# Kernel tuning notes

Hardware: AMD Instinct MI355X
Metric: run time of the kernel (lower is better)

Reference implementation:

```python
import jax, jax.numpy as jnp
import numpy as np

N_NODES = 50000
N_EDGES = 500000
H = 128          # h_dim
HEADS = 3
B = 512          # histories with non-zero length
L = 10           # seq_len (all histories full length)
N_RELS = 200
NEG_SLOPE = 0.2  # DGL GATConv default negative_slope


def setup_inputs() -> dict:
    key = jax.random.key(0)
    ks = jax.random.split(key, 18)
    p = lambda i, shape: jax.random.normal(ks[i], shape, jnp.float32) * 0.05
    return {
        "node_feat": jax.random.normal(ks[0], (N_NODES, H), jnp.float32),
        "W1": p(1, (H, HEADS * H)),
        "attn_l1": p(2, (HEADS, H)),
        "attn_r1": p(3, (HEADS, H)),
        "b1": p(4, (HEADS * H,)),
        "W2": p(5, (H, HEADS * H)),
        "attn_l2": p(6, (HEADS, H)),
        "attn_r2": p(7, (HEADS, H)),
        "b2": p(8, (HEADS * H,)),
        "ent_embeds": jax.random.normal(ks[9], (N_NODES, H), jnp.float32),
        "rel_embeds": jax.random.normal(ks[10], (N_RELS, H), jnp.float32),
        "global_emb_list": jax.random.normal(ks[11], (B * L, H), jnp.float32),
        "s_hist_t": jax.random.uniform(ks[12], (B, L), jnp.float32),
        "edge_src": jax.random.randint(ks[13], (N_EDGES,), 0, N_NODES),
        "edge_dst": jax.random.randint(ks[14], (N_EDGES,), 0, N_NODES),
        "node_ids_graph": jax.random.randint(ks[15], (B * L,), 0, N_NODES),
        "s_tem": jax.random.randint(ks[16], (B,), 0, N_NODES),
        "r_tem": jax.random.randint(ks[17], (B,), 0, N_RELS),
    }


def gat_conv(x, W, attn_l, attn_r, bias, src, dst):
    """DGL-style GATConv (allow_zero_in_degree=True, eval mode)."""
    n = x.shape[0]
    feat = (x @ W).reshape(n, HEADS, H)                    # [N, heads, H]
    el = jnp.einsum('nhd,hd->nh', feat, attn_l)            # [N, heads]
    er = jnp.einsum('nhd,hd->nh', feat, attn_r)
    e = jax.nn.leaky_relu(el[src] + er[dst], NEG_SLOPE)    # [E, heads]
    # edge softmax over incoming edges of each dst node
    emax = jax.ops.segment_max(e, dst, num_segments=n)
    ex = jnp.exp(e - emax[dst])
    denom = jax.ops.segment_sum(ex, dst, num_segments=n)
    alpha = ex / denom[dst]                                # [E, heads]
    msg = alpha[:, :, None] * feat[src]                    # [E, heads, H]
    rst = jax.ops.segment_sum(msg, dst, num_segments=n)    # [N, heads, H]
    return rst + bias.reshape(1, HEADS, H)


def reference(node_feat, W1, attn_l1, attn_r1, b1, W2, attn_l2, attn_r2, b2,
              ent_embeds, rel_embeds, global_emb_list, s_hist_t,
              edge_src, edge_dst, node_ids_graph, s_tem, r_tem):
    h = gat_conv(node_feat, W1, attn_l1, attn_r1, b1, edge_src, edge_dst).mean(axis=1)
    h = gat_conv(h, W2, attn_l2, attn_r2, b2, edge_src, edge_dst).mean(axis=1)
    embeds = h[node_ids_graph].reshape(B, L, H)            # gathered history node embeds
    ent = jnp.broadcast_to(ent_embeds[s_tem][:, None, :], (B, L, H))
    rel = jnp.broadcast_to(rel_embeds[r_tem][:, None, :], (B, L, H))
    glob = global_emb_list.reshape(B, L, H)
    seq = jnp.concatenate([embeds, ent, rel, glob], axis=-1)   # [B, L, 4H]
    seq_r = jnp.concatenate([embeds, ent, glob], axis=-1)      # [B, L, 3H]
    return seq, seq_r, s_hist_t
```

## Files before the change

### kernel.cpp

```cpp
#include <hip/hip_runtime.h>
#include <hip/hip_bf16.h>

#define N_NODES 50000
#define N_EDGES 500000
#define HDIM 128
#define HEADS 3
#define BB 512
#define LL 10
#define NEG_SLOPE 0.2f

typedef __hip_bfloat16 bf16;
typedef unsigned char fp8t;
typedef __bf16 v8bf __attribute__((ext_vector_type(8)));
typedef float f32x4 __attribute__((ext_vector_type(4)));


__global__ void k_zero1(int* a, int n){
  int i = blockIdx.x*256 + threadIdx.x;
  if(i < n) a[i] = 0;
}

__global__ void k_hist(const int* __restrict__ dst, int* __restrict__ cnt, int E){
  int e = blockIdx.x*256 + threadIdx.x;
  if(e < E) atomicAdd(&cnt[dst[e]], 1);
}


#define SCAN_TILE 2048
#define SCAN_NB ((N_NODES + SCAN_TILE - 1)/SCAN_TILE)

__global__ __launch_bounds__(256) void k_scan_part(const int* __restrict__ cnt,
                                                   int* __restrict__ bsum){
  int b = blockIdx.x, tid = threadIdx.x;
  int i0 = b*SCAN_TILE + tid*8;
  int s = 0;
  #pragma unroll
  for(int j = 0; j < 8; ++j){ int i = i0 + j; s += (i < N_NODES) ? cnt[i] : 0; }
  for(int m = 32; m; m >>= 1) s += __shfl_xor(s, m);
  __shared__ int ws[4];
  if((tid & 63) == 0) ws[tid >> 6] = s;
  __syncthreads();
  if(tid == 0) bsum[b] = ws[0] + ws[1] + ws[2] + ws[3];
}

__global__ __launch_bounds__(64) void k_scan_top(int* __restrict__ bsum, int nb){
  int tid = threadIdx.x;
  int v = (tid < nb) ? bsum[tid] : 0;
  for(int s = 1; s < 64; s <<= 1){
    int t = __shfl_up(v, s);
    if(tid >= s) v += t;
  }
  if(tid < nb) bsum[tid] = v;
}

__global__ __launch_bounds__(256) void k_scan_write(int* __restrict__ cnt,
                                                    const int* __restrict__ bsum,
                                                    int* __restrict__ offs){
  int b = blockIdx.x, tid = threadIdx.x;
  int lane = tid & 63, wv = tid >> 6;
  int i0 = b*SCAN_TILE + tid*8;
  int v[8]; int s = 0;
  #pragma unroll
  for(int j = 0; j < 8; ++j){
    int i = i0 + j;
    v[j] = (i < N_NODES) ? cnt[i] : 0;
    s += v[j];
  }
  #pragma unroll
  for(int j = 0; j < 8; ++j){ int i = i0 + j; if(i < N_NODES) cnt[i] = 0; }
  int incl = s;
  for(int sh = 1; sh < 64; sh <<= 1){
    int t = __shfl_up(incl, sh);
    if(lane >= sh) incl += t;
  }
  __shared__ int wtot[4];
  if(lane == 63) wtot[wv] = incl;
  __syncthreads();
  int woff = 0;
  for(int w = 0; w < wv; ++w) woff += wtot[w];
  int excl = woff + incl - s;
  int run = ((b > 0) ? bsum[b-1] : 0) + excl;
  #pragma unroll
  for(int j = 0; j < 8; ++j){
    int i = i0 + j;
    run += v[j];
    if(i < N_NODES) offs[i+1] = run;
  }
  if(b == 0 && tid == 0) offs[0] = 0;
}

__global__ void k_scatter(const int* __restrict__ src, const int* __restrict__ dst,
                          const int* __restrict__ offs, int* __restrict__ cur,
                          int* __restrict__ csr, int E){
  int e = blockIdx.x*256 + threadIdx.x;
  if(e < E){
    int d = dst[e];
    int p = offs[d] + atomicAdd(&cur[d], 1);
    if(p >= 0 && p < E) csr[p] = src[e];
  }
}


__global__ void k_wt(const float* __restrict__ W, bf16* __restrict__ Wt){
  int i = blockIdx.x*256 + threadIdx.x;
  if(i < HEADS*HDIM*HDIM){
    int n = i >> 7, k = i & 127;
    Wt[i] = __float2bfloat16(W[k*(HEADS*HDIM) + n]);
  }
}


template<int AF32>
__global__ __launch_bounds__(256) void k_gemm(const void* __restrict__ Av,
                                              const bf16* __restrict__ Wt,
                                              const float* __restrict__ al,
                                              const float* __restrict__ ar,
                                              fp8t* __restrict__ feat8,
                                              float* __restrict__ el,
                                              float* __restrict__ er, int M){
  int tid  = threadIdx.x;
  int wave = tid >> 6, lane = tid & 63;
  int wr = wave >> 1, wc = wave & 1;
  int row0 = blockIdx.x*64 + wr*32;
  int col0 = blockIdx.y*128 + wc*64;
  int l15 = lane & 15, lhi = lane >> 4;

  f32x4 acc[2][4] = {};
  for(int kk = 0; kk < 4; ++kk){
    int kb = kk*32 + lhi*8;
    v8bf a[2], b[4];
    for(int mi = 0; mi < 2; ++mi){
      int r = row0 + mi*16 + l15;
      if(r >= M) r = M - 1;
      if constexpr(AF32){
        const float* ap = (const float*)Av + (size_t)r*HDIM + kb;
        f32x4 lo = *reinterpret_cast<const f32x4*>(ap);
        f32x4 hi = *reinterpret_cast<const f32x4*>(ap + 4);
        #pragma unroll
        for(int j = 0; j < 4; ++j){ a[mi][j] = (__bf16)lo[j]; a[mi][4+j] = (__bf16)hi[j]; }
      } else {
        a[mi] = *reinterpret_cast<const v8bf*>((const bf16*)Av + (size_t)r*HDIM + kb);
      }
    }
    for(int ni = 0; ni < 4; ++ni){
      int c = col0 + ni*16 + l15;
      b[ni] = *reinterpret_cast<const v8bf*>(Wt + (size_t)c*HDIM + kb);
    }
    for(int mi = 0; mi < 2; ++mi)
      for(int ni = 0; ni < 4; ++ni)
        acc[mi][ni] = __builtin_amdgcn_mfma_f32_16x16x32_bf16(a[mi], b[ni], acc[mi][ni], 0, 0, 0);
  }

  const float* alh = al + blockIdx.y*HDIM;
  const float* arh = ar + blockIdx.y*HDIM;
  float alv[4], arv[4];
  #pragma unroll
  for(int ni = 0; ni < 4; ++ni){
    int d = wc*64 + ni*16 + l15;
    alv[ni] = alh[d]; arv[ni] = arh[d];
  }
  __shared__ float red[2][64][2];
  __shared__ int4 tile4[512];
  fp8t* tile8 = (fp8t*)tile4;

  #pragma unroll
  for(int mi = 0; mi < 2; ++mi){
    #pragma unroll
    for(int j = 0; j < 4; ++j){
      float pe = 0.f, pr = 0.f;
      #pragma unroll
      for(int ni = 0; ni < 4; ++ni){
        pe += acc[mi][ni][j]*alv[ni];
        pr += acc[mi][ni][j]*arv[ni];
      }
      for(int k = 8; k; k >>= 1){ pe += __shfl_xor(pe, k); pr += __shfl_xor(pr, k); }
      int row_l = wr*32 + mi*16 + lhi*4 + j;
      if(l15 == 0){ red[wc][row_l][0] = pe; red[wc][row_l][1] = pr; }
    }
  }
  #pragma unroll
  for(int mi = 0; mi < 2; ++mi)
    #pragma unroll
    for(int j = 0; j < 4; ++j){
      int row_l = wr*32 + mi*16 + lhi*4 + j;
      #pragma unroll
      for(int ni = 0; ni < 4; ++ni){
        float x = acc[mi][ni][j];
        unsigned bb = (unsigned)__builtin_amdgcn_cvt_pk_fp8_f32(x, x, 0, false) & 0xFFu;
        tile8[row_l*128 + wc*64 + ni*16 + l15] = (fp8t)bb;
      }
    }
  __syncthreads();

  if(tid < 64){
    int r = blockIdx.x*64 + tid;
    if(r < M){
      el[r*3 + blockIdx.y] = red[0][tid][0] + red[1][tid][0];
      er[r*3 + blockIdx.y] = red[0][tid][1] + red[1][tid][1];
    }
  }
  #pragma unroll
  for(int pass = 0; pass < 2; ++pass){
    int off = pass*4096 + tid*16;
    int row_l = off >> 7, col = off & 127;
    int r = blockIdx.x*64 + row_l;
    if(r < M)
      *reinterpret_cast<int4*>(feat8 + (size_t)r*(HEADS*HDIM) + blockIdx.y*HDIM + col) =
          tile4[off >> 4];
  }
}


__device__ __forceinline__ float lrelu(float x){ return x > 0.f ? x : NEG_SLOPE*x; }
__device__ __forceinline__ float cvt8(fp8t b){
  return __builtin_amdgcn_cvt_f32_fp8((int)b, 0);
}

#define AGG_CHUNK 128

template<int USE_LIST, int OUT_F32>
__global__ __launch_bounds__(128) void k_agg(const fp8t* __restrict__ feat8,
                                             const float* __restrict__ el,
                                             const float* __restrict__ er,
                                             const float* __restrict__ bias,
                                             const int* __restrict__ offs,
                                             const int* __restrict__ csr,
                                             const int* __restrict__ list,
                                             void* __restrict__ hout){
  int bid = blockIdx.x;
  int n = USE_LIST ? list[bid] : bid;
  int tid = threadIdx.x, lane = tid & 63, wv = tid >> 6;
  __shared__ float s_m[2][3], s_s[2][3];
  __shared__ float s_alpha[AGG_CHUNK][4];
  __shared__ int   s_src[AGG_CHUNK];
  int o0 = offs[n];
  int deg = offs[n+1] - o0;
  if(deg < 0 || deg > N_EDGES) deg = 0;
  float er0 = er[n*3+0], er1 = er[n*3+1], er2 = er[n*3+2];

  float M0 = -1e30f, M1 = -1e30f, M2 = -1e30f;
  float S0 = 0.f, S1 = 0.f, S2 = 0.f;
  float cx0 = 0.f, cx1 = 0.f, cx2 = 0.f; int cs = 0;

  for(int base = 0; base < deg; base += AGG_CHUNK){
    int cn = min(AGG_CHUNK, deg - base);
    float x0 = -1e30f, x1 = -1e30f, x2 = -1e30f; int s = 0;
    if(tid < cn){
      unsigned su = (unsigned)csr[o0 + base + tid];
      if(su >= N_NODES) su = 0;
      s = (int)su;
      x0 = lrelu(el[s*3+0] + er0);
      x1 = lrelu(el[s*3+1] + er1);
      x2 = lrelu(el[s*3+2] + er2);
    }
    if(base == 0){ cx0 = x0; cx1 = x1; cx2 = x2; cs = s; }
    float m0 = x0, m1 = x1, m2 = x2;
    for(int k = 32; k; k >>= 1){
      m0 = fmaxf(m0, __shfl_xor(m0, k));
      m1 = fmaxf(m1, __shfl_xor(m1, k));
      m2 = fmaxf(m2, __shfl_xor(m2, k));
    }
    if(lane == 0){ s_m[wv][0] = m0; s_m[wv][1] = m1; s_m[wv][2] = m2; }
    __syncthreads();
    float nm0 = fmaxf(M0, fmaxf(s_m[0][0], s_m[1][0]));
    float nm1 = fmaxf(M1, fmaxf(s_m[0][1], s_m[1][1]));
    float nm2 = fmaxf(M2, fmaxf(s_m[0][2], s_m[1][2]));
    float e0 = (tid < cn) ? __expf(x0 - nm0) : 0.f;
    float e1 = (tid < cn) ? __expf(x1 - nm1) : 0.f;
    float e2 = (tid < cn) ? __expf(x2 - nm2) : 0.f;
    for(int k = 32; k; k >>= 1){
      e0 += __shfl_xor(e0, k); e1 += __shfl_xor(e1, k); e2 += __shfl_xor(e2, k);
    }
    if(lane == 0){ s_s[wv][0] = e0; s_s[wv][1] = e1; s_s[wv][2] = e2; }
    __syncthreads();
    S0 = S0*__expf(M0 - nm0) + s_s[0][0] + s_s[1][0];
    S1 = S1*__expf(M1 - nm1) + s_s[0][1] + s_s[1][1];
    S2 = S2*__expf(M2 - nm2) + s_s[0][2] + s_s[1][2];
    M0 = nm0; M1 = nm1; M2 = nm2;
  }
  float i0 = 1.f/S0, i1 = 1.f/S1, i2 = 1.f/S2;

  float a0 = 0.f, a1 = 0.f, a2 = 0.f;
  for(int base = 0; base < deg; base += AGG_CHUNK){
    int cn = min(AGG_CHUNK, deg - base);
    __syncthreads();
    if(tid < cn){
      int s; float x0, x1, x2;
      if(base == 0){ s = cs; x0 = cx0; x1 = cx1; x2 = cx2; }
      else {
        unsigned su = (unsigned)csr[o0 + base + tid];
        if(su >= N_NODES) su = 0;
        s = (int)su;
        x0 = lrelu(el[s*3+0] + er0);
        x1 = lrelu(el[s*3+1] + er1);
        x2 = lrelu(el[s*3+2] + er2);
      }
      s_src[tid] = s;
      s_alpha[tid][0] = __expf(x0 - M0)*i0;
      s_alpha[tid][1] = __expf(x1 - M1)*i1;
      s_alpha[tid][2] = __expf(x2 - M2)*i2;
    }
    __syncthreads();
    for(int i = 0; i < cn; ++i){
      const fp8t* fr = feat8 + (size_t)s_src[i]*(HEADS*HDIM);
      float al0 = s_alpha[i][0], al1 = s_alpha[i][1], al2 = s_alpha[i][2];
      a0 += al0*cvt8(fr[tid]);
      a1 += al1*cvt8(fr[HDIM + tid]);
      a2 += al2*cvt8(fr[2*HDIM + tid]);
    }
  }
  float r = (a0 + a1 + a2 + bias[tid] + bias[HDIM+tid] + bias[2*HDIM+tid])*(1.f/3.f);
  if(OUT_F32) ((float*)hout)[(size_t)bid*HDIM + tid] = r;
  else        ((bf16*)hout)[(size_t)bid*HDIM + tid] = __float2bfloat16(r);
}


#define SEQ_SZ   (BB*LL*4*HDIM)
#define SEQR_OFF SEQ_SZ
#define SEQR_SZ  (BB*LL*3*HDIM)
#define SH_OFF   (SEQ_SZ + SEQR_SZ)

__global__ __launch_bounds__(128) void k_assemble(const float* __restrict__ h2s,
                                                  const float* __restrict__ ent_e,
                                                  const float* __restrict__ rel_e,
                                                  const float* __restrict__ glob,
                                                  const float* __restrict__ sht,
                                                  const int* __restrict__ s_tem,
                                                  const int* __restrict__ r_tem,
                                                  float* __restrict__ out){
  int p = blockIdx.x;
  int d = threadIdx.x;
  int b = p / LL;
  float emb = h2s[(size_t)p*HDIM + d];
  float ent = ent_e[(size_t)s_tem[b]*HDIM + d];
  float rel = rel_e[(size_t)r_tem[b]*HDIM + d];
  float gl  = glob[(size_t)p*HDIM + d];
  size_t so = (size_t)p*(4*HDIM);
  out[so + d] = emb; out[so + HDIM + d] = ent;
  out[so + 2*HDIM + d] = rel; out[so + 3*HDIM + d] = gl;
  size_t ro = SEQR_OFF + (size_t)p*(3*HDIM);
  out[ro + d] = emb; out[ro + HDIM + d] = ent; out[ro + 2*HDIM + d] = gl;
  if(d == 0) out[SH_OFF + p] = sht[p];
}


extern "C" void kernel_launch(void* const* d_in, const int* in_sizes, int n_in,
                              void* d_out, int out_size, void* d_ws, size_t ws_size,
                              hipStream_t stream){
  const float* node_feat = (const float*)d_in[0];
  const float* W1        = (const float*)d_in[1];
  const float* attn_l1   = (const float*)d_in[2];
  const float* attn_r1   = (const float*)d_in[3];
  const float* b1        = (const float*)d_in[4];
  const float* W2        = (const float*)d_in[5];
  const float* attn_l2   = (const float*)d_in[6];
  const float* attn_r2   = (const float*)d_in[7];
  const float* b2        = (const float*)d_in[8];
  const float* ent_emb   = (const float*)d_in[9];
  const float* rel_emb   = (const float*)d_in[10];
  const float* glob      = (const float*)d_in[11];
  const float* sht       = (const float*)d_in[12];
  const int*  e_src      = (const int*)d_in[13];
  const int*  e_dst      = (const int*)d_in[14];
  const int*  nid        = (const int*)d_in[15];
  const int*  s_tem      = (const int*)d_in[16];
  const int*  r_tem      = (const int*)d_in[17];
  float* out = (float*)d_out;

  char* ws = (char*)d_ws;
  size_t cur_off = 0;
  auto alloc = [&](size_t bytes)->char*{
    char* r = ws + cur_off;
    cur_off += (bytes + 255) & ~(size_t)255;
    return r;
  };
  fp8t*  feat8 = (fp8t*) alloc((size_t)N_NODES*HEADS*HDIM);
  bf16*  h1    = (bf16*) alloc((size_t)N_NODES*HDIM*2);
  float* h2s   = (float*)alloc((size_t)BB*LL*HDIM*4);
  float* el    = (float*)alloc((size_t)N_NODES*HEADS*4);
  float* er    = (float*)alloc((size_t)N_NODES*HEADS*4);
  bf16*  wt1   = (bf16*) alloc((size_t)HEADS*HDIM*HDIM*2);
  bf16*  wt2   = (bf16*) alloc((size_t)HEADS*HDIM*HDIM*2);
  int*   offs  = (int*)  alloc((size_t)(N_NODES+1)*4);
  int*   cnt   = (int*)  alloc((size_t)N_NODES*4);
  int*   bsum  = (int*)  alloc((size_t)SCAN_NB*4);
  int*   csr   = (int*)  alloc((size_t)N_EDGES*4);

  k_zero1<<<(N_NODES+255)/256, 256, 0, stream>>>(cnt, N_NODES);
  k_hist<<<(N_EDGES+255)/256, 256, 0, stream>>>(e_dst, cnt, N_EDGES);
  k_scan_part<<<SCAN_NB, 256, 0, stream>>>(cnt, bsum);
  k_scan_top<<<1, 64, 0, stream>>>(bsum, SCAN_NB);
  k_scan_write<<<SCAN_NB, 256, 0, stream>>>(cnt, bsum, offs);
  k_scatter<<<(N_EDGES+255)/256, 256, 0, stream>>>(e_src, e_dst, offs, cnt, csr, N_EDGES);

  k_wt<<<(HEADS*HDIM*HDIM+255)/256, 256, 0, stream>>>(W1, wt1);
  k_wt<<<(HEADS*HDIM*HDIM+255)/256, 256, 0, stream>>>(W2, wt2);

  dim3 ggrid((N_NODES + 63)/64, HEADS);

  k_gemm<1><<<ggrid, 256, 0, stream>>>((const void*)node_feat, wt1, attn_l1, attn_r1,
                                       feat8, el, er, N_NODES);
  k_agg<0,0><<<N_NODES, 128, 0, stream>>>(feat8, el, er, b1, offs, csr, nullptr, (void*)h1);

  k_gemm<0><<<ggrid, 256, 0, stream>>>((const void*)h1, wt2, attn_l2, attn_r2,
                                       feat8, el, er, N_NODES);
  k_agg<1,1><<<BB*LL, 128, 0, stream>>>(feat8, el, er, b2, offs, csr, nid, (void*)h2s);

  k_assemble<<<BB*LL, 128, 0, stream>>>(h2s, ent_emb, rel_emb, glob, sht,
                                        s_tem, r_tem, out);
}
```

Measured before the change: 229.4 us.

## Prune layer-1 aggregation to needed nodes and add single-chunk fast path

A new k_mark kernel flags the history nodes and their in-neighbours. Only those nodes are needed by the second GAT layer for the gathered outputs, so the layer-1 aggregation exits early for every unmarked node and that share of edge-gather work is skipped. The el/er arrays are padded to four floats per node so the attention logits can be read with one vector load. A fast path for nodes with degree ≤128 computes the softmax in a single pass, and 96 threads each accumulate four fp8 features from one 32-bit load. The costs are an extra marking kernel and uninitialised h1 rows for unmarked nodes. The second GEMM still reads those rows, but their results are never consumed.

```diff
diff --git a/kernel.cpp b/kernel.cpp
--- a/kernel.cpp
+++ b/kernel.cpp
@@ -15,9 +15,10 @@
 typedef float f32x4 __attribute__((ext_vector_type(4)));
 
 
-__global__ void k_zero1(int* a, int n){
+__global__ void k_zero2(int* a, int na, int* b, int nb){
   int i = blockIdx.x*256 + threadIdx.x;
-  if(i < n) a[i] = 0;
+  if(i < na) a[i] = 0;
+  if(i < nb) b[i] = 0;
 }
 
 __global__ void k_hist(const int* __restrict__ dst, int* __restrict__ cnt, int E){
@@ -101,6 +102,21 @@
 }
 
 
+__global__ __launch_bounds__(64) void k_mark(const int* __restrict__ nid,
+                                             const int* __restrict__ offs,
+                                             const int* __restrict__ csr,
+                                             unsigned char* __restrict__ mark){
+  unsigned n = (unsigned)nid[blockIdx.x];
+  if(n >= N_NODES) return;
+  if(threadIdx.x == 0) mark[n] = 1;
+  int o0 = offs[n], o1 = offs[n+1];
+  for(int j = o0 + (int)threadIdx.x; j < o1; j += 64){
+    unsigned s = (unsigned)csr[j];
+    if(s < N_NODES) mark[s] = 1;
+  }
+}
+
+
 __global__ void k_wt(const float* __restrict__ W, bf16* __restrict__ Wt){
   int i = blockIdx.x*256 + threadIdx.x;
   if(i < HEADS*HDIM*HDIM){
@@ -116,8 +132,8 @@
                                               const float* __restrict__ al,
                                               const float* __restrict__ ar,
                                               fp8t* __restrict__ feat8,
-                                              float* __restrict__ el,
-                                              float* __restrict__ er, int M){
+                                              float* __restrict__ el4,
+                                              float* __restrict__ er4, int M){
   int tid  = threadIdx.x;
   int wave = tid >> 6, lane = tid & 63;
   int wr = wave >> 1, wc = wave & 1;
@@ -195,8 +211,8 @@
   if(tid < 64){
     int r = blockIdx.x*64 + tid;
     if(r < M){
-      el[r*3 + blockIdx.y] = red[0][tid][0] + red[1][tid][0];
-      er[r*3 + blockIdx.y] = red[0][tid][1] + red[1][tid][1];
+      el4[(size_t)r*4 + blockIdx.y] = red[0][tid][0] + red[1][tid][0];
+      er4[(size_t)r*4 + blockIdx.y] = red[0][tid][1] + red[1][tid][1];
     }
   }
   #pragma unroll
@@ -218,42 +234,102 @@
 
 #define AGG_CHUNK 128
 
-template<int USE_LIST, int OUT_F32>
+template<int USE_LIST, int OUT_F32, int USE_MARK>
 __global__ __launch_bounds__(128) void k_agg(const fp8t* __restrict__ feat8,
-                                             const float* __restrict__ el,
-                                             const float* __restrict__ er,
+                                             const float* __restrict__ el4,
+                                             const float* __restrict__ er4,
                                              const float* __restrict__ bias,
                                              const int* __restrict__ offs,
                                              const int* __restrict__ csr,
                                              const int* __restrict__ list,
+                                             const unsigned char* __restrict__ mark,
                                              void* __restrict__ hout){
   int bid = blockIdx.x;
   int n = USE_LIST ? list[bid] : bid;
+  if(USE_MARK){ if(!mark[n]) return; }
   int tid = threadIdx.x, lane = tid & 63, wv = tid >> 6;
   __shared__ float s_m[2][3], s_s[2][3];
   __shared__ float s_alpha[AGG_CHUNK][4];
   __shared__ int   s_src[AGG_CHUNK];
+  __shared__ float s_facc[HEADS*HDIM];
   int o0 = offs[n];
   int deg = offs[n+1] - o0;
   if(deg < 0 || deg > N_EDGES) deg = 0;
-  float er0 = er[n*3+0], er1 = er[n*3+1], er2 = er[n*3+2];
+  float4 erv = *reinterpret_cast<const float4*>(er4 + (size_t)n*4);
+
+  if(deg <= AGG_CHUNK){
+    float x0 = -1e30f, x1 = -1e30f, x2 = -1e30f; int s = 0;
+    if(tid < deg){
+      unsigned su = (unsigned)csr[o0 + tid];
+      if(su >= N_NODES) su = 0;
+      s = (int)su;
+      float4 elv = *reinterpret_cast<const float4*>(el4 + (size_t)s*4);
+      x0 = lrelu(elv.x + erv.x);
+      x1 = lrelu(elv.y + erv.y);
+      x2 = lrelu(elv.z + erv.z);
+    }
+    float m0 = x0, m1 = x1, m2 = x2;
+    for(int k = 32; k; k >>= 1){
+      m0 = fmaxf(m0, __shfl_xor(m0, k));
+      m1 = fmaxf(m1, __shfl_xor(m1, k));
+      m2 = fmaxf(m2, __shfl_xor(m2, k));
+    }
+    if(lane == 0){ s_m[wv][0] = m0; s_m[wv][1] = m1; s_m[wv][2] = m2; }
+    __syncthreads();
+    m0 = fmaxf(s_m[0][0], s_m[1][0]);
+    m1 = fmaxf(s_m[0][1], s_m[1][1]);
+    m2 = fmaxf(s_m[0][2], s_m[1][2]);
+    float e0 = (tid < deg) ? __expf(x0 - m0) : 0.f;
+    float e1 = (tid < deg) ? __expf(x1 - m1) : 0.f;
+    float e2 = (tid < deg) ? __expf(x2 - m2) : 0.f;
+    float t0 = e0, t1 = e1, t2 = e2;
+    for(int k = 32; k; k >>= 1){
+      t0 += __shfl_xor(t0, k); t1 += __shfl_xor(t1, k); t2 += __shfl_xor(t2, k);
+    }
+    if(lane == 0){ s_s[wv][0] = t0; s_s[wv][1] = t1; s_s[wv][2] = t2; }
+    if(tid < deg){
+      s_src[tid] = s;
+      s_alpha[tid][0] = e0; s_alpha[tid][1] = e1; s_alpha[tid][2] = e2;
+    }
+    __syncthreads();
+    if(tid < 96){
+      int head = tid >> 5;
+      float S = s_s[0][head] + s_s[1][head];
+      float ih = (S > 0.f) ? 1.f/S : 0.f;
+      float a0 = 0.f, a1 = 0.f, a2 = 0.f, a3 = 0.f;
+      for(int i = 0; i < deg; ++i){
+        unsigned u = *reinterpret_cast<const unsigned*>(
+            feat8 + (size_t)s_src[i]*(HEADS*HDIM) + tid*4);
+        float al = s_alpha[i][head];
+        a0 += al*__builtin_amdgcn_cvt_f32_fp8((int)u, 0);
+        a1 += al*__builtin_amdgcn_cvt_f32_fp8((int)u, 1);
+        a2 += al*__builtin_amdgcn_cvt_f32_fp8((int)u, 2);
+        a3 += al*__builtin_amdgcn_cvt_f32_fp8((int)u, 3);
+      }
+      float4 w; w.x = a0*ih; w.y = a1*ih; w.z = a2*ih; w.w = a3*ih;
+      *reinterpret_cast<float4*>(s_facc + tid*4) = w;
+    }
+    __syncthreads();
+    float r = (s_facc[tid] + s_facc[HDIM + tid] + s_facc[2*HDIM + tid]
+             + bias[tid] + bias[HDIM + tid] + bias[2*HDIM + tid])*(1.f/3.f);
+    if(OUT_F32) ((float*)hout)[(size_t)bid*HDIM + tid] = r;
+    else        ((bf16*)hout)[(size_t)bid*HDIM + tid] = __float2bfloat16(r);
+    return;
+  }
 
   float M0 = -1e30f, M1 = -1e30f, M2 = -1e30f;
   float S0 = 0.f, S1 = 0.f, S2 = 0.f;
-  float cx0 = 0.f, cx1 = 0.f, cx2 = 0.f; int cs = 0;
-
   for(int base = 0; base < deg; base += AGG_CHUNK){
     int cn = min(AGG_CHUNK, deg - base);
-    float x0 = -1e30f, x1 = -1e30f, x2 = -1e30f; int s = 0;
+    float x0 = -1e30f, x1 = -1e30f, x2 = -1e30f;
     if(tid < cn){
       unsigned su = (unsigned)csr[o0 + base + tid];
       if(su >= N_NODES) su = 0;
-      s = (int)su;
-      x0 = lrelu(el[s*3+0] + er0);
-      x1 = lrelu(el[s*3+1] + er1);
-      x2 = lrelu(el[s*3+2] + er2);
-    }
-    if(base == 0){ cx0 = x0; cx1 = x1; cx2 = x2; cs = s; }
+      float4 elv = *reinterpret_cast<const float4*>(el4 + (size_t)su*4);
+      x0 = lrelu(elv.x + erv.x);
+      x1 = lrelu(elv.y + erv.y);
+      x2 = lrelu(elv.z + erv.z);
+    }
     float m0 = x0, m1 = x1, m2 = x2;
     for(int k = 32; k; k >>= 1){
       m0 = fmaxf(m0, __shfl_xor(m0, k));
@@ -268,10 +344,11 @@
     float e0 = (tid < cn) ? __expf(x0 - nm0) : 0.f;
     float e1 = (tid < cn) ? __expf(x1 - nm1) : 0.f;
     float e2 = (tid < cn) ? __expf(x2 - nm2) : 0.f;
+    float t0 = e0, t1 = e1, t2 = e2;
     for(int k = 32; k; k >>= 1){
-      e0 += __shfl_xor(e0, k); e1 += __shfl_xor(e1, k); e2 += __shfl_xor(e2, k);
-    }
-    if(lane == 0){ s_s[wv][0] = e0; s_s[wv][1] = e1; s_s[wv][2] = e2; }
+      t0 += __shfl_xor(t0, k); t1 += __shfl_xor(t1, k); t2 += __shfl_xor(t2, k);
+    }
+    if(lane == 0){ s_s[wv][0] = t0; s_s[wv][1] = t1; s_s[wv][2] = t2; }
     __syncthreads();
     S0 = S0*__expf(M0 - nm0) + s_s[0][0] + s_s[1][0];
     S1 = S1*__expf(M1 - nm1) + s_s[0][1] + s_s[1][1];
@@ -285,28 +362,20 @@
     int cn = min(AGG_CHUNK, deg - base);
     __syncthreads();
     if(tid < cn){
-      int s; float x0, x1, x2;
-      if(base == 0){ s = cs; x0 = cx0; x1 = cx1; x2 = cx2; }
-      else {
-        unsigned su = (unsigned)csr[o0 + base + tid];
-        if(su >= N_NODES) su = 0;
-        s = (int)su;
-        x0 = lrelu(el[s*3+0] + er0);
-        x1 = lrelu(el[s*3+1] + er1);
-        x2 = lrelu(el[s*3+2] + er2);
-      }
-      s_src[tid] = s;
-      s_alpha[tid][0] = __expf(x0 - M0)*i0;
-      s_alpha[tid][1] = __expf(x1 - M1)*i1;
-      s_alpha[tid][2] = __expf(x2 - M2)*i2;
+      unsigned su = (unsigned)csr[o0 + base + tid];
+      if(su >= N_NODES) su = 0;
+      float4 elv = *reinterpret_cast<const float4*>(el4 + (size_t)su*4);
+      s_src[tid] = (int)su;
+      s_alpha[tid][0] = __expf(lrelu(elv.x + erv.x) - M0)*i0;
+      s_alpha[tid][1] = __expf(lrelu(elv.y + erv.y) - M1)*i1;
+      s_alpha[tid][2] = __expf(lrelu(elv.z + erv.z) - M2)*i2;
     }
     __syncthreads();
     for(int i = 0; i < cn; ++i){
       const fp8t* fr = feat8 + (size_t)s_src[i]*(HEADS*HDIM);
-      float al0 = s_alpha[i][0], al1 = s_alpha[i][1], al2 = s_alpha[i][2];
-      a0 += al0*cvt8(fr[tid]);
-      a1 += al1*cvt8(fr[HDIM + tid]);
-      a2 += al2*cvt8(fr[2*HDIM + tid]);
+      a0 += s_alpha[i][0]*cvt8(fr[tid]);
+      a1 += s_alpha[i][1]*cvt8(fr[HDIM + tid]);
+      a2 += s_alpha[i][2]*cvt8(fr[2*HDIM + tid]);
     }
   }
   float r = (a0 + a1 + a2 + bias[tid] + bias[HDIM+tid] + bias[2*HDIM+tid])*(1.f/3.f);
@@ -377,21 +446,24 @@
   fp8t*  feat8 = (fp8t*) alloc((size_t)N_NODES*HEADS*HDIM);
   bf16*  h1    = (bf16*) alloc((size_t)N_NODES*HDIM*2);
   float* h2s   = (float*)alloc((size_t)BB*LL*HDIM*4);
-  float* el    = (float*)alloc((size_t)N_NODES*HEADS*4);
-  float* er    = (float*)alloc((size_t)N_NODES*HEADS*4);
+  float* el4   = (float*)alloc((size_t)N_NODES*4*4);
+  float* er4   = (float*)alloc((size_t)N_NODES*4*4);
   bf16*  wt1   = (bf16*) alloc((size_t)HEADS*HDIM*HDIM*2);
   bf16*  wt2   = (bf16*) alloc((size_t)HEADS*HDIM*HDIM*2);
   int*   offs  = (int*)  alloc((size_t)(N_NODES+1)*4);
   int*   cnt   = (int*)  alloc((size_t)N_NODES*4);
   int*   bsum  = (int*)  alloc((size_t)SCAN_NB*4);
+  unsigned char* mark = (unsigned char*)alloc((size_t)N_NODES);
   int*   csr   = (int*)  alloc((size_t)N_EDGES*4);
 
-  k_zero1<<<(N_NODES+255)/256, 256, 0, stream>>>(cnt, N_NODES);
+  k_zero2<<<(N_NODES+255)/256, 256, 0, stream>>>(cnt, N_NODES,
+                                                 (int*)mark, (N_NODES+3)/4);
   k_hist<<<(N_EDGES+255)/256, 256, 0, stream>>>(e_dst, cnt, N_EDGES);
   k_scan_part<<<SCAN_NB, 256, 0, stream>>>(cnt, bsum);
   k_scan_top<<<1, 64, 0, stream>>>(bsum, SCAN_NB);
   k_scan_write<<<SCAN_NB, 256, 0, stream>>>(cnt, bsum, offs);
   k_scatter<<<(N_EDGES+255)/256, 256, 0, stream>>>(e_src, e_dst, offs, cnt, csr, N_EDGES);
+  k_mark<<<BB*LL, 64, 0, stream>>>(nid, offs, csr, mark);
 
   k_wt<<<(HEADS*HDIM*HDIM+255)/256, 256, 0, stream>>>(W1, wt1);
   k_wt<<<(HEADS*HDIM*HDIM+255)/256, 256, 0, stream>>>(W2, wt2);
@@ -399,12 +471,14 @@
   dim3 ggrid((N_NODES + 63)/64, HEADS);
 
   k_gemm<1><<<ggrid, 256, 0, stream>>>((const void*)node_feat, wt1, attn_l1, attn_r1,
-                                       feat8, el, er, N_NODES);
-  k_agg<0,0><<<N_NODES, 128, 0, stream>>>(feat8, el, er, b1, offs, csr, nullptr, (void*)h1);
+                                       feat8, el4, er4, N_NODES);
+  k_agg<0,0,1><<<N_NODES, 128, 0, stream>>>(feat8, el4, er4, b1, offs, csr,
+                                            nullptr, mark, (void*)h1);
 
   k_gemm<0><<<ggrid, 256, 0, stream>>>((const void*)h1, wt2, attn_l2, attn_r2,
-                                       feat8, el, er, N_NODES);
-  k_agg<1,1><<<BB*LL, 128, 0, stream>>>(feat8, el, er, b2, offs, csr, nid, (void*)h2s);
+                                       feat8, el4, er4, N_NODES);
+  k_agg<1,1,0><<<BB*LL, 128, 0, stream>>>(feat8, el4, er4, b2, offs, csr,
+                                          nid, nullptr, (void*)h2s);
 
   k_assemble<<<BB*LL, 128, 0, stream>>>(h2s, ent_emb, rel_emb, glob, sht,
                                         s_tem, r_tem, out);
```

After: 212.8 us. 7.2% less time.
